# Kernel optimization log

Measured on AMD Instinct MI355X. Metric: run time of the kernel, lower is better.

## Reference

```python
import jax, jax.numpy as jnp
import numpy as np


def _gru_dirs(x, h, w_ih, w_hh, b_ih, b_hh):
    # One GRU step for both directions at once (seq_len==1 per original loop).
    # x: [N, in], h: [2, N, H]; w_ih: [2, 3H, in], w_hh: [2, 3H, H], biases [2, 3H]
    gi = jnp.einsum('ni,dgi->dng', x, w_ih) + b_ih[:, None, :]
    gh = jnp.einsum('dnh,dgh->dng', h, w_hh) + b_hh[:, None, :]
    H = h.shape[-1]
    ir, iz, inn = gi[..., :H], gi[..., H:2 * H], gi[..., 2 * H:]
    hr, hz, hn = gh[..., :H], gh[..., H:2 * H], gh[..., 2 * H:]
    r = jax.nn.sigmoid(ir + hr)
    z = jax.nn.sigmoid(iz + hz)
    n = jnp.tanh(inn + r * hn)
    return (1.0 - z) * n + z * h


def setup_inputs() -> dict:
    key = jax.random.key(0)
    ks = jax.random.split(key, 6)
    V, E, H, NL = 32000, 1024, 512, 2  # vocab, input_size, hidden_size, num_layers
    N, L = 32, 512
    s = 0.05
    x = jax.random.randint(ks[0], (N, L), 0, V)
    emb = jax.random.normal(ks[1], (V, E), dtype=jnp.float32) * s
    w_ih = jax.random.normal(ks[2], (NL, 2, 3 * H, E), dtype=jnp.float32) * s
    w_hh = jax.random.normal(ks[3], (NL, 2, 3 * H, H), dtype=jnp.float32) * s
    b_ih = jax.random.normal(ks[4], (NL, 2, 3 * H), dtype=jnp.float32) * s
    b_hh = jax.random.normal(ks[5], (NL, 2, 3 * H), dtype=jnp.float32) * s
    return {"x": x, "emb": emb, "w_ih": w_ih, "w_hh": w_hh, "b_ih": b_ih, "b_hh": b_hh}


def reference(x, emb, w_ih, w_hh, b_ih, b_hh):
    # Because the torch code calls the bidirectional GRU one timestep at a time
    # with a carried hidden, BOTH directions scan left-to-right over the sequence.
    N, L = x.shape
    num_layers = w_ih.shape[0]
    H = w_hh.shape[-1]
    h0 = jnp.zeros((num_layers, 2, N, H), dtype=emb.dtype)

    def step(h, xt):
        layer_in = emb[xt]  # [N, E] embedding lookup for this timestep
        new_h = []
        for l in range(num_layers):  # fixed small layer loop
            hl = _gru_dirs(layer_in, h[l], w_ih[l], w_hh[l], b_ih[l], b_hh[l])
            new_h.append(hl)
            layer_in = jnp.concatenate([hl[0], hl[1]], axis=-1)  # [N, 2H]
        hs = jnp.stack(new_h)  # [num_layers, 2, N, H]
        return hs, (layer_in, hs)

    _, (outs, hiddens) = jax.lax.scan(step, h0, x.T)  # scan over L timesteps
    outputs = jnp.transpose(outs, (1, 0, 2))  # [N, L, 2H]
    hiddens = hiddens.reshape(L, num_layers * 2, N, H)  # [L, 2*num_layers, N, H]
    return outputs, hiddens
```

## Files before the change

### kernel.cpp

```cpp
#include <hip/hip_runtime.h>
#include <hip/hip_bf16.h>

using u16 = unsigned short;
using u32 = unsigned int;
using bf16x8 = __attribute__((ext_vector_type(8))) __bf16;
using f32x4  = __attribute__((ext_vector_type(4))) float;

#define GLP(p) ((const __attribute__((address_space(1))) void*)(p))
#define LDSP(p) ((__attribute__((address_space(3))) void*)(p))

__device__ __forceinline__ float bf2f(u16 u) {
    union { float f; u32 i; } v; v.i = ((u32)u) << 16; return v.f;
}
__device__ __forceinline__ u16 f2bf(float f) {
    union { float f; u32 i; } v; v.f = f;
    u32 r = v.i + 0x7FFFu + ((v.i >> 16) & 1u);
    return (u16)(r >> 16);
}

__device__ __forceinline__ u32 ld_sc01_u32(const u32* p) {
    u32 v;
    asm volatile("global_load_dword %0, %1, off sc0 sc1\n\ts_waitcnt vmcnt(0)"
                 : "=v"(v) : "v"(p) : "memory");
    return v;
}
__device__ __forceinline__ void st_sc01_u32(u32* p, u32 v) {
    asm volatile("global_store_dword %0, %1, off sc0 sc1" :: "v"(p), "v"(v) : "memory");
}
__device__ __forceinline__ void st_sc01_u16(u16* p, u16 v) {
    asm volatile("global_store_short %0, %1, off sc0 sc1" :: "v"(p), "v"(v) : "memory");
}

__global__ void k_gather(const int* __restrict__ x, const float* __restrict__ emb,
                         u16* __restrict__ X0) {
    int gid = blockIdx.x * blockDim.x + threadIdx.x;
    if (gid >= 16384 * 256) return;
    int e4 = gid << 2;
    int m = e4 >> 10, k = e4 & 1023;
    int t = m >> 5, n = m & 31;
    int tok = x[n * 512 + t];
    float4 v = *reinterpret_cast<const float4*>(emb + ((size_t)tok << 10) + k);
    ushort4 o;
    o.x = f2bf(v.x); o.y = f2bf(v.y); o.z = f2bf(v.z); o.w = f2bf(v.w);
    *reinterpret_cast<ushort4*>(X0 + (size_t)e4) = o;
}

__global__ void k_f32bf16(const float* __restrict__ s, u16* __restrict__ d, int n4) {
    int gid = blockIdx.x * blockDim.x + threadIdx.x;
    if (gid >= n4) return;
    float4 v = reinterpret_cast<const float4*>(s)[gid];
    ushort4 o;
    o.x = f2bf(v.x); o.y = f2bf(v.y); o.z = f2bf(v.z); o.w = f2bf(v.w);
    reinterpret_cast<ushort4*>(d)[gid] = o;
}

__global__ __launch_bounds__(256) void k_gemm(const u16* __restrict__ A,
                                              const u16* __restrict__ B,
                                              const float* __restrict__ bias,
                                              u16* __restrict__ C,
                                              int M, int N, int K) {
    __shared__ __align__(16) u16 As[128 * 64];
    __shared__ __align__(16) u16 Bs[128 * 64];
    const int tid = threadIdx.x;
    const int lane = tid & 63, wid = tid >> 6;
    const int wm = wid >> 1, wn = wid & 1;
    const int m0 = blockIdx.y * 128, n0 = blockIdx.x * 128;
    const int lr = lane & 15, lk = lane >> 4;
    f32x4 zero = {0.f, 0.f, 0.f, 0.f};
    f32x4 acc[4][4];
    #pragma unroll
    for (int i = 0; i < 4; ++i)
        #pragma unroll
        for (int j = 0; j < 4; ++j) acc[i][j] = zero;

    for (int k0 = 0; k0 < K; k0 += 64) {
        #pragma unroll
        for (int r = 0; r < 4; ++r) {
            int c = wid * 4 + r;
            int o = c * 1024 + lane * 16;
            int row = o >> 7;
            int kb = o & 127;
            int kbs = kb ^ ((row & 7) << 4);
            const char* sa = (const char*)A + ((size_t)(m0 + row) * K + k0) * 2 + kbs;
            const char* sb = (const char*)B + ((size_t)(n0 + row) * K + k0) * 2 + kbs;
            __builtin_amdgcn_global_load_lds(GLP(sa), LDSP((char*)As + c * 1024), 16, 0, 0);
            __builtin_amdgcn_global_load_lds(GLP(sb), LDSP((char*)Bs + c * 1024), 16, 0, 0);
        }
        __syncthreads();
        #pragma unroll
        for (int kk = 0; kk < 2; ++kk) {
            bf16x8 af[4], bfr[4];
            #pragma unroll
            for (int i = 0; i < 4; ++i) {
                int rowA = wm * 64 + i * 16 + lr;
                int rowB = wn * 64 + i * 16 + lr;
                int kb = kk * 64 + lk * 16;
                af[i]  = *reinterpret_cast<const bf16x8*>((const char*)As + rowA * 128 + (kb ^ ((rowA & 7) << 4)));
                bfr[i] = *reinterpret_cast<const bf16x8*>((const char*)Bs + rowB * 128 + (kb ^ ((rowB & 7) << 4)));
            }
            #pragma unroll
            for (int i = 0; i < 4; ++i)
                #pragma unroll
                for (int j = 0; j < 4; ++j)
                    acc[i][j] = __builtin_amdgcn_mfma_f32_16x16x32_bf16(af[i], bfr[j], acc[i][j], 0, 0, 0);
        }
        __syncthreads();
    }
    #pragma unroll
    for (int j = 0; j < 4; ++j) {
        int col = n0 + wn * 64 + j * 16 + lr;
        float bv = bias[col];
        #pragma unroll
        for (int i = 0; i < 4; ++i) {
            int rowb = m0 + wm * 64 + i * 16 + lk * 4;
            #pragma unroll
            for (int q = 0; q < 4; ++q)
                C[(size_t)(rowb + q) * N + col] = f2bf(acc[i][j][q] + bv);
        }
    }
}

template<int LAYER>
__device__ __forceinline__ void gru_body(char* smem, int d, int wg,
    const u16* __restrict__ Gi, const u16* __restrict__ Whh_l,
    const float* __restrict__ bhh_l, u16* __restrict__ hbuf,
    u16* __restrict__ X1, float* __restrict__ hid, float* __restrict__ outp,
    u32* __restrict__ flags, u32* __restrict__ xflags, const u32* __restrict__ gdone)
{
    char* hS          = smem;
    float (*ghs)[196] = (float(*)[196])(smem + 32768);
    u16 (*gis)[208]   = (u16(*)[208])(smem + 57856);
    float* bhh_s      = (float*)(smem + 71168);
    const int tid = threadIdx.x;
    const int lane = tid & 63, w = tid >> 6;
    const int j0 = wg * 64;
    const int g = w >> 2, joff = (w & 3) * 16;
    const int lr = lane & 15, lk = lane >> 4;

    if (tid < 192) {
        int g2 = tid >> 6, jj = tid & 63;
        bhh_s[tid] = bhh_l[d * 1536 + g2 * 512 + j0 + jj];
    }
    bf16x8 wf[16];
    {
        const u16* wr = Whh_l + (size_t)(d * 1536 + g * 512 + j0 + joff + lr) * 512 + lk * 8;
        #pragma unroll
        for (int kt = 0; kt < 16; ++kt)
            wf[kt] = *reinterpret_cast<const bf16x8*>(wr + kt * 32);
    }
    if (LAYER == 1 && tid == 0) {
        long long T0 = __builtin_amdgcn_s_memrealtime();
        while (ld_sc01_u32(&gdone[0]) == 0) {
            __builtin_amdgcn_s_sleep(4);
            if (__builtin_amdgcn_s_memrealtime() - T0 > 2000000) break;
        }
    }
    __syncthreads();

    const int p_nb = tid / 24, p_gc = tid % 24;
    const int p_lg = p_gc * 8;
    const int p_col = d * 1536 + (p_lg >> 6) * 512 + j0 + (p_lg & 63);
    const u32* myflags = flags + d * 8 * 32;
    u32* myflag  = flags  + (d * 8 + wg) * 32;
    u32* myxflag = (LAYER == 0) ? xflags + (d * 8 + wg) * 32 : nullptr;

    float hp0 = 0.f, hp1 = 0.f, hp2 = 0.f;
    uint4 gv;
    if (LAYER == 0)
        gv = *reinterpret_cast<const uint4*>(Gi + (size_t)p_nb * 3072 + p_col);

    for (int t = 0; t < 512; ++t) {
        if (t > 0) {
            if (tid < 8) {
                const u32* fp = myflags + tid * 32;
                long long tt0 = __builtin_amdgcn_s_memrealtime();
                while (ld_sc01_u32(fp) < (u32)t) {
                    __builtin_amdgcn_s_sleep(1);
                    if (__builtin_amdgcn_s_memrealtime() - tt0 > 2000) {
                        __hip_atomic_store(myflag, (u32)t, __ATOMIC_RELEASE,
                                           __HIP_MEMORY_SCOPE_AGENT);
                        tt0 = __builtin_amdgcn_s_memrealtime();
                    }
                }
            } else if (LAYER == 1 && tid == 8) {
                long long tt0 = __builtin_amdgcn_s_memrealtime();
                while (ld_sc01_u32(&gdone[t >> 2]) == 0) {
                    __builtin_amdgcn_s_sleep(1);
                    if (__builtin_amdgcn_s_memrealtime() - tt0 > 2000000) break;
                }
            }
            __syncthreads();
        }

        const u16* hb = hbuf + ((size_t)d * 2 + ((t + 1) & 1)) * 16384;
        uint4 hv0, hv1, hv2;
        {
            int c0 = tid, c1 = tid + 768, c2 = tid + 1536;
            asm volatile("global_load_dwordx4 %0, %1, off sc0 sc1"
                         : "=v"(hv0) : "v"(hb + (size_t)(c0 >> 6) * 512 + (c0 & 63) * 8));
            asm volatile("global_load_dwordx4 %0, %1, off sc0 sc1"
                         : "=v"(hv1) : "v"(hb + (size_t)(c1 >> 6) * 512 + (c1 & 63) * 8));
            if (c2 < 2048)
                asm volatile("global_load_dwordx4 %0, %1, off sc0 sc1"
                             : "=v"(hv2) : "v"(hb + (size_t)(c2 >> 6) * 512 + (c2 & 63) * 8));
        }
        if (LAYER == 1) {
            const u16* gip = Gi + (size_t)(t * 32 + p_nb) * 3072 + p_col;
            asm volatile("global_load_dwordx4 %0, %1, off sc0 sc1" : "=v"(gv) : "v"(gip));
        }
        asm volatile("s_waitcnt vmcnt(0)" ::: "memory");
        {
            int c0 = tid, c1 = tid + 768, c2 = tid + 1536;
            int r0 = c0 >> 6, r1 = c1 >> 6, r2 = c2 >> 6;
            *reinterpret_cast<uint4*>(hS + r0 * 1024 + (((c0 & 63) * 16) ^ ((r0 & 15) << 4))) = hv0;
            *reinterpret_cast<uint4*>(hS + r1 * 1024 + (((c1 & 63) * 16) ^ ((r1 & 15) << 4))) = hv1;
            if (c2 < 2048)
                *reinterpret_cast<uint4*>(hS + r2 * 1024 + (((c2 & 63) * 16) ^ ((r2 & 15) << 4))) = hv2;
        }
        *reinterpret_cast<uint4*>(&gis[p_nb][p_lg]) = gv;
        __syncthreads();

        f32x4 acc0 = {0.f, 0.f, 0.f, 0.f}, acc1 = acc0;
        #pragma unroll
        for (int ktb = 0; ktb < 4; ++ktb) {
            bf16x8 a0[4], a1[4];
            #pragma unroll
            for (int r = 0; r < 4; ++r) {
                int kt = ktb * 4 + r;
                int boff = (lk * 16 + kt * 64) ^ (lr << 4);
                a0[r] = *reinterpret_cast<const bf16x8*>(hS + lr * 1024 + boff);
                a1[r] = *reinterpret_cast<const bf16x8*>(hS + (16 + lr) * 1024 + boff);
            }
            #pragma unroll
            for (int r = 0; r < 4; ++r) {
                acc0 = __builtin_amdgcn_mfma_f32_16x16x32_bf16(a0[r], wf[ktb * 4 + r], acc0, 0, 0, 0);
                acc1 = __builtin_amdgcn_mfma_f32_16x16x32_bf16(a1[r], wf[ktb * 4 + r], acc1, 0, 0, 0);
            }
        }
        int colg = w * 16 + lr;
        float bv = bhh_s[colg];
        #pragma unroll
        for (int q = 0; q < 4; ++q) {
            ghs[lk * 4 + q][colg]      = acc0[q] + bv;
            ghs[16 + lk * 4 + q][colg] = acc1[q] + bv;
        }
        if (LAYER == 0) {
            int tn = (t + 1 < 512) ? t + 1 : t;
            gv = *reinterpret_cast<const uint4*>(Gi + (size_t)(tn * 32 + p_nb) * 3072 + p_col);
        }
        __syncthreads();

        u16* hbw = hbuf + ((size_t)d * 2 + (t & 1)) * 16384;
        #pragma unroll
        for (int rep = 0; rep < 3; ++rep) {
            int e = tid + rep * 768;
            if (e < 2048) {
                int j = e & 63, nb = e >> 6;
                float gr = bf2f(gis[nb][j])       + ghs[nb][j];
                float gz = bf2f(gis[nb][64 + j])  + ghs[nb][64 + j];
                float r = 1.f / (1.f + __expf(-gr));
                float z = 1.f / (1.f + __expf(-gz));
                float ng = tanhf(bf2f(gis[nb][128 + j]) + r * ghs[nb][128 + j]);
                float hp = (rep == 0) ? hp0 : (rep == 1) ? hp1 : hp2;
                float hv = (1.f - z) * ng + z * hp;
                if (rep == 0) hp0 = hv; else if (rep == 1) hp1 = hv; else hp2 = hv;
                st_sc01_u16(hbw + (size_t)nb * 512 + j0 + j, f2bf(hv));
            }
        }
        asm volatile("s_waitcnt vmcnt(0)" ::: "memory");
        __syncthreads();
        if (tid == 0)
            st_sc01_u32(myflag, (u32)(t + 1));

        #pragma unroll
        for (int rep = 0; rep < 3; ++rep) {
            int e = tid + rep * 768;
            if (e < 2048) {
                int j = e & 63, nb = e >> 6;
                float hv = (rep == 0) ? hp0 : (rep == 1) ? hp1 : hp2;
                hid[((size_t)(t * 4 + LAYER * 2 + d) * 32 + nb) * 512 + j0 + j] = hv;
                if (LAYER == 0)
                    st_sc01_u16(X1 + ((size_t)(t * 32 + nb)) * 1024 + (size_t)d * 512 + j0 + j,
                                f2bf(hv));
                else
                    outp[((size_t)nb * 512 + t) * 1024 + (size_t)d * 512 + j0 + j] = hv;
            }
        }
        if (LAYER == 0) {
            asm volatile("s_waitcnt vmcnt(0)" ::: "memory");
            __syncthreads();
            if (tid == 0)
                st_sc01_u32(myxflag, (u32)(t + 1));
        }
    }
}

__device__ __forceinline__ void chaser_body(char* smem, int w,
    const u16* __restrict__ X1, const u16* __restrict__ Wih1,
    const float* __restrict__ bih1, u16* __restrict__ Gi,
    const u32* __restrict__ xflags, u32* __restrict__ cnt, u32* __restrict__ gdone)
{
    u16* As = (u16*)smem;
    u16* Bs = (u16*)(smem + 16384);
    const int tid = threadIdx.x;
    const int lane = tid & 63, wid = tid >> 6;
    const int wm = wid & 1, wn = wid >> 1;
    const int lr = lane & 15, lk = lane >> 4;
    const int x = w & 31, yg = w >> 5;

    for (int y = yg; y < 128; y += 3) {
        if (tid < 16) {
            const u32* fp = xflags + tid * 32;
            u32 target = 4u * (u32)y + 4u;
            long long T0 = __builtin_amdgcn_s_memrealtime();
            while (ld_sc01_u32(fp) < target) {
                __builtin_amdgcn_s_sleep(4);
                if (__builtin_amdgcn_s_memrealtime() - T0 > 2000000) break;
            }
        }
        __syncthreads();

        f32x4 zero = {0.f, 0.f, 0.f, 0.f};
        f32x4 acc[4][2];
        #pragma unroll
        for (int i = 0; i < 4; ++i) { acc[i][0] = zero; acc[i][1] = zero; }

        for (int k0 = 0; k0 < 1024; k0 += 64) {
            #pragma unroll
            for (int r = 0; r < 5; ++r) {
                int c = wid * 5 + r;
                if (c < 16) {
                    int o = c * 1024 + lane * 16;
                    int row = o >> 7, kb = o & 127;
                    int kbs = kb ^ ((row & 7) << 4);
                    const char* s = (const char*)X1 + ((size_t)(y * 128 + row) * 1024 + k0) * 2 + kbs;
                    __builtin_amdgcn_global_load_lds(GLP(s), LDSP((char*)As + c * 1024), 16, 0, 0);
                } else if (c < 28) {
                    int c2 = c - 16;
                    int o = c2 * 1024 + lane * 16;
                    int row = o >> 7, kb = o & 127;
                    int kbs = kb ^ ((row & 7) << 4);
                    const char* s = (const char*)Wih1 + ((size_t)(x * 96 + row) * 1024 + k0) * 2 + kbs;
                    __builtin_amdgcn_global_load_lds(GLP(s), LDSP((char*)Bs + c2 * 1024), 16, 0, 0);
                }
            }
            __syncthreads();
            if (wid < 6) {
                #pragma unroll
                for (int kk = 0; kk < 2; ++kk) {
                    bf16x8 af[4], bfr[2];
                    int kb = kk * 64 + lk * 16;
                    #pragma unroll
                    for (int i = 0; i < 4; ++i) {
                        int rowA = wm * 64 + i * 16 + lr;
                        af[i] = *reinterpret_cast<const bf16x8*>((const char*)As + rowA * 128 + (kb ^ ((rowA & 7) << 4)));
                    }
                    #pragma unroll
                    for (int j = 0; j < 2; ++j) {
                        int rowB = wn * 32 + j * 16 + lr;
                        bfr[j] = *reinterpret_cast<const bf16x8*>((const char*)Bs + rowB * 128 + (kb ^ ((rowB & 7) << 4)));
                    }
                    #pragma unroll
                    for (int i = 0; i < 4; ++i)
                        #pragma unroll
                        for (int j = 0; j < 2; ++j)
                            acc[i][j] = __builtin_amdgcn_mfma_f32_16x16x32_bf16(af[i], bfr[j], acc[i][j], 0, 0, 0);
                }
            }
            __syncthreads();
        }
        if (wid < 6) {
            #pragma unroll
            for (int j = 0; j < 2; ++j) {
                int col = x * 96 + wn * 32 + j * 16 + lr;
                float bv = bih1[col];
                #pragma unroll
                for (int i = 0; i < 4; ++i) {
                    int rowb = y * 128 + wm * 64 + i * 16 + lk * 4;
                    #pragma unroll
                    for (int q = 0; q < 4; ++q)
                        st_sc01_u16(Gi + (size_t)(rowb + q) * 3072 + col, f2bf(acc[i][j][q] + bv));
                }
            }
        }
        asm volatile("s_waitcnt vmcnt(0)" ::: "memory");
        __syncthreads();
        if (tid == 0) {
            u32 old = __hip_atomic_fetch_add(&cnt[y], 1u, __ATOMIC_RELAXED,
                                             __HIP_MEMORY_SCOPE_AGENT);
            if (old == 31u)
                st_sc01_u32(&gdone[y], 1u);
        }
    }
}

__global__ __launch_bounds__(768, 3) void k_fused(
    const u16* __restrict__ Gi_r, u16* __restrict__ Gi_w,
    const u16* __restrict__ Whh, const float* __restrict__ bhh,
    u16* __restrict__ hbuf0, u16* __restrict__ hbuf1,
    u16* __restrict__ X1, const u16* __restrict__ Wih1, const float* __restrict__ bih1,
    float* __restrict__ hid, float* __restrict__ outp,
    u32* __restrict__ flags0, u32* __restrict__ flags1,
    u32* __restrict__ xflags, u32* __restrict__ cnt, u32* __restrict__ gdone)
{
    __shared__ __align__(16) char smem[71936];
    int bid = blockIdx.x;
    if (bid < 16) {
        gru_body<0>(smem, bid >> 3, bid & 7, Gi_r, Whh, bhh, hbuf0,
                    X1, hid, outp, flags0, xflags, nullptr);
    } else if (bid < 112) {
        chaser_body(smem, bid - 16, X1, Wih1, bih1, Gi_w, xflags, cnt, gdone);
    } else {
        int b = bid - 112;
        gru_body<1>(smem, b >> 3, b & 7, Gi_r, Whh + (size_t)3072 * 512, bhh + 3072,
                    hbuf1, nullptr, hid, outp, flags1, nullptr, gdone);
    }
}

extern "C" void kernel_launch(void* const* d_in, const int* in_sizes, int n_in,
                              void* d_out, int out_size, void* d_ws, size_t ws_size,
                              hipStream_t stream) {
    const int*   x    = (const int*)d_in[0];
    const float* emb  = (const float*)d_in[1];
    const float* w_ih = (const float*)d_in[2];
    const float* w_hh = (const float*)d_in[3];
    const float* b_ih = (const float*)d_in[4];
    const float* b_hh = (const float*)d_in[5];
    float* outp = (float*)d_out;
    float* hid  = outp + (size_t)32 * 512 * 1024;

    char* ws = (char*)d_ws;
    u16* X0     = (u16*)(ws);
    u16* X1     = (u16*)(ws + 33554432);
    u16* Wih    = (u16*)(ws + 67108864);
    u16* Whh    = (u16*)(ws + 79691776);
    u16* Gi     = (u16*)(ws + 85983232);
    u16* hbuf0  = (u16*)(ws + 186646528);
    u16* hbuf1  = (u16*)(ws + 186777600);
    u32* flags0 = (u32*)(ws + 186908672);
    u32* flags1 = (u32*)(ws + 186910720);
    u32* xflags = (u32*)(ws + 186912768);
    u32* cnt    = (u32*)(ws + 186914816);
    u32* gdone  = (u32*)(ws + 186915328);

    k_gather<<<16384, 256, 0, stream>>>(x, emb, X0);
    k_f32bf16<<<(1572864 + 255) / 256, 256, 0, stream>>>(w_ih, Wih, 1572864);
    k_f32bf16<<<( 786432 + 255) / 256, 256, 0, stream>>>(w_hh, Whh, 786432);

    hipMemsetAsync(hbuf0, 0, 269312, stream);

    k_gemm<<<dim3(24, 128), 256, 0, stream>>>(X0, Wih, b_ih, Gi, 16384, 3072, 1024);

    k_fused<<<128, 768, 0, stream>>>(Gi, Gi, Whh, b_hh, hbuf0, hbuf1,
                                     X1, Wih + (size_t)3072 * 1024, b_ih + 3072,
                                     hid, outp, flags0, flags1, xflags, cnt, gdone);
}
```

Before: 2.396 ms.

## Split hidden-state load to overlap MFMA with loads and vectorize output stores

```diff
diff --git a/kernel.cpp b/kernel.cpp
--- a/kernel.cpp
+++ b/kernel.cpp
@@ -5,6 +5,7 @@
 using u32 = unsigned int;
 using bf16x8 = __attribute__((ext_vector_type(8))) __bf16;
 using f32x4  = __attribute__((ext_vector_type(4))) float;
+using u32x4  = __attribute__((ext_vector_type(4))) u32;
 
 #define GLP(p) ((const __attribute__((address_space(1))) void*)(p))
 #define LDSP(p) ((__attribute__((address_space(3))) void*)(p))
@@ -29,6 +30,9 @@
 }
 __device__ __forceinline__ void st_sc01_u16(u16* p, u16 v) {
     asm volatile("global_store_short %0, %1, off sc0 sc1" :: "v"(p), "v"(v) : "memory");
+}
+__device__ __forceinline__ void st_sc01_u32x4(u16* p, u32x4 v) {
+    asm volatile("global_store_dwordx4 %0, %1, off sc0 sc1" :: "v"(p), "v"(v) : "memory");
 }
 
 __global__ void k_gather(const int* __restrict__ x, const float* __restrict__ emb,
@@ -131,6 +135,7 @@
     float (*ghs)[196] = (float(*)[196])(smem + 32768);
     u16 (*gis)[208]   = (u16(*)[208])(smem + 57856);
     float* bhh_s      = (float*)(smem + 71168);
+    u16* hvS          = (u16*)(smem + 71936);
     const int tid = threadIdx.x;
     const int lane = tid & 63, w = tid >> 6;
     const int j0 = wg * 64;
@@ -163,6 +168,10 @@
     const u32* myflags = flags + d * 8 * 32;
     u32* myflag  = flags  + (d * 8 + wg) * 32;
     u32* myxflag = (LAYER == 0) ? xflags + (d * 8 + wg) * 32 : nullptr;
+
+    const int srow = tid >> 6;
+    const int scol = (tid & 63) * 8;
+    const int scb  = (tid & 63) * 16;
 
     float hp0 = 0.f, hp1 = 0.f, hp2 = 0.f;
     uint4 gv;
@@ -193,49 +202,58 @@
         }
 
         const u16* hb = hbuf + ((size_t)d * 2 + ((t + 1) & 1)) * 16384;
-        uint4 hv0, hv1, hv2;
-        {
-            int c0 = tid, c1 = tid + 768, c2 = tid + 1536;
+        u32x4 va0, va1, vb0, vb1, gvv;
+        if (tid < 512) {
             asm volatile("global_load_dwordx4 %0, %1, off sc0 sc1"
-                         : "=v"(hv0) : "v"(hb + (size_t)(c0 >> 6) * 512 + (c0 & 63) * 8));
+                         : "=v"(va0) : "v"(hb + (size_t)srow * 512 + scol));
             asm volatile("global_load_dwordx4 %0, %1, off sc0 sc1"
-                         : "=v"(hv1) : "v"(hb + (size_t)(c1 >> 6) * 512 + (c1 & 63) * 8));
-            if (c2 < 2048)
-                asm volatile("global_load_dwordx4 %0, %1, off sc0 sc1"
-                             : "=v"(hv2) : "v"(hb + (size_t)(c2 >> 6) * 512 + (c2 & 63) * 8));
+                         : "=v"(va1) : "v"(hb + (size_t)(srow + 8) * 512 + scol));
+            asm volatile("global_load_dwordx4 %0, %1, off sc0 sc1"
+                         : "=v"(vb0) : "v"(hb + (size_t)(srow + 16) * 512 + scol));
+            asm volatile("global_load_dwordx4 %0, %1, off sc0 sc1"
+                         : "=v"(vb1) : "v"(hb + (size_t)(srow + 24) * 512 + scol));
         }
         if (LAYER == 1) {
             const u16* gip = Gi + (size_t)(t * 32 + p_nb) * 3072 + p_col;
-            asm volatile("global_load_dwordx4 %0, %1, off sc0 sc1" : "=v"(gv) : "v"(gip));
-        }
-        asm volatile("s_waitcnt vmcnt(0)" ::: "memory");
-        {
-            int c0 = tid, c1 = tid + 768, c2 = tid + 1536;
-            int r0 = c0 >> 6, r1 = c1 >> 6, r2 = c2 >> 6;
-            *reinterpret_cast<uint4*>(hS + r0 * 1024 + (((c0 & 63) * 16) ^ ((r0 & 15) << 4))) = hv0;
-            *reinterpret_cast<uint4*>(hS + r1 * 1024 + (((c1 & 63) * 16) ^ ((r1 & 15) << 4))) = hv1;
-            if (c2 < 2048)
-                *reinterpret_cast<uint4*>(hS + r2 * 1024 + (((c2 & 63) * 16) ^ ((r2 & 15) << 4))) = hv2;
-        }
-        *reinterpret_cast<uint4*>(&gis[p_nb][p_lg]) = gv;
-        __syncthreads();
-
-        f32x4 acc0 = {0.f, 0.f, 0.f, 0.f}, acc1 = acc0;
-        #pragma unroll
-        for (int ktb = 0; ktb < 4; ++ktb) {
-            bf16x8 a0[4], a1[4];
-            #pragma unroll
-            for (int r = 0; r < 4; ++r) {
-                int kt = ktb * 4 + r;
-                int boff = (lk * 16 + kt * 64) ^ (lr << 4);
-                a0[r] = *reinterpret_cast<const bf16x8*>(hS + lr * 1024 + boff);
-                a1[r] = *reinterpret_cast<const bf16x8*>(hS + (16 + lr) * 1024 + boff);
-            }
-            #pragma unroll
-            for (int r = 0; r < 4; ++r) {
-                acc0 = __builtin_amdgcn_mfma_f32_16x16x32_bf16(a0[r], wf[ktb * 4 + r], acc0, 0, 0, 0);
-                acc1 = __builtin_amdgcn_mfma_f32_16x16x32_bf16(a1[r], wf[ktb * 4 + r], acc1, 0, 0, 0);
-            }
+            asm volatile("global_load_dwordx4 %0, %1, off sc0 sc1" : "=v"(gvv) : "v"(gip));
+        }
+        if (tid < 512) {
+            if (LAYER == 0) asm volatile("s_waitcnt vmcnt(2)" ::: "memory");
+            else            asm volatile("s_waitcnt vmcnt(3)" ::: "memory");
+            int r0 = srow, r1 = srow + 8;
+            *reinterpret_cast<u32x4*>(hS + r0 * 1024 + (scb ^ ((r0 & 15) << 4))) = va0;
+            *reinterpret_cast<u32x4*>(hS + r1 * 1024 + (scb ^ ((r1 & 15) << 4))) = va1;
+        }
+        __syncthreads();
+
+        f32x4 acc0 = {0.f, 0.f, 0.f, 0.f};
+        #pragma unroll
+        for (int kt = 0; kt < 16; ++kt) {
+            int boff = (lk * 16 + kt * 64) ^ (lr << 4);
+            bf16x8 a = *reinterpret_cast<const bf16x8*>(hS + lr * 1024 + boff);
+            acc0 = __builtin_amdgcn_mfma_f32_16x16x32_bf16(a, wf[kt], acc0, 0, 0, 0);
+        }
+        if (tid < 512) {
+            asm volatile("s_waitcnt vmcnt(0)" ::: "memory");
+            int r2 = srow + 16, r3 = srow + 24;
+            *reinterpret_cast<u32x4*>(hS + r2 * 1024 + (scb ^ ((r2 & 15) << 4))) = vb0;
+            *reinterpret_cast<u32x4*>(hS + r3 * 1024 + (scb ^ ((r3 & 15) << 4))) = vb1;
+        } else if (LAYER == 1) {
+            asm volatile("s_waitcnt vmcnt(0)" ::: "memory");
+        }
+        if (LAYER == 0) {
+            *reinterpret_cast<uint4*>(&gis[p_nb][p_lg]) = gv;
+        } else {
+            *reinterpret_cast<u32x4*>(&gis[p_nb][p_lg]) = gvv;
+        }
+        __syncthreads();
+
+        f32x4 acc1 = {0.f, 0.f, 0.f, 0.f};
+        #pragma unroll
+        for (int kt = 0; kt < 16; ++kt) {
+            int boff = (lk * 16 + kt * 64) ^ (lr << 4);
+            bf16x8 a = *reinterpret_cast<const bf16x8*>(hS + (16 + lr) * 1024 + boff);
+            acc1 = __builtin_amdgcn_mfma_f32_16x16x32_bf16(a, wf[kt], acc1, 0, 0, 0);
         }
         int colg = w * 16 + lr;
         float bv = bhh_s[colg];
@@ -264,32 +282,38 @@
                 float hp = (rep == 0) ? hp0 : (rep == 1) ? hp1 : hp2;
                 float hv = (1.f - z) * ng + z * hp;
                 if (rep == 0) hp0 = hv; else if (rep == 1) hp1 = hv; else hp2 = hv;
-                st_sc01_u16(hbw + (size_t)nb * 512 + j0 + j, f2bf(hv));
+                u16 hb16 = f2bf(hv);
+                st_sc01_u16(hbw + (size_t)nb * 512 + j0 + j, hb16);
+                hvS[nb * 64 + j] = hb16;
             }
         }
         asm volatile("s_waitcnt vmcnt(0)" ::: "memory");
         __syncthreads();
-        if (tid == 0)
+        if (tid == 16)
             st_sc01_u32(myflag, (u32)(t + 1));
 
-        #pragma unroll
-        for (int rep = 0; rep < 3; ++rep) {
-            int e = tid + rep * 768;
-            if (e < 2048) {
-                int j = e & 63, nb = e >> 6;
-                float hv = (rep == 0) ? hp0 : (rep == 1) ? hp1 : hp2;
-                hid[((size_t)(t * 4 + LAYER * 2 + d) * 32 + nb) * 512 + j0 + j] = hv;
-                if (LAYER == 0)
-                    st_sc01_u16(X1 + ((size_t)(t * 32 + nb)) * 1024 + (size_t)d * 512 + j0 + j,
-                                f2bf(hv));
-                else
-                    outp[((size_t)nb * 512 + t) * 1024 + (size_t)d * 512 + j0 + j] = hv;
-            }
-        }
-        if (LAYER == 0) {
+        if (tid >= 512) {
+            int q = tid - 512, nb = q >> 3, j8 = (q & 7) * 8;
+            union { u32x4 v; u16 s[8]; } h8;
+            h8.v = *reinterpret_cast<const u32x4*>(hvS + nb * 64 + j8);
+            float f0 = bf2f(h8.s[0]), f1 = bf2f(h8.s[1]), f2 = bf2f(h8.s[2]), f3 = bf2f(h8.s[3]);
+            float f4 = bf2f(h8.s[4]), f5 = bf2f(h8.s[5]), f6 = bf2f(h8.s[6]), f7 = bf2f(h8.s[7]);
+            float* hp = hid + ((size_t)(t * 4 + LAYER * 2 + d) * 32 + nb) * 512 + j0 + j8;
+            *reinterpret_cast<float4*>(hp)     = make_float4(f0, f1, f2, f3);
+            *reinterpret_cast<float4*>(hp + 4) = make_float4(f4, f5, f6, f7);
+            if (LAYER == 0) {
+                u16* xp = X1 + (size_t)(t * 32 + nb) * 1024 + (size_t)d * 512 + j0 + j8;
+                st_sc01_u32x4(xp, h8.v);
+            } else {
+                float* op = outp + ((size_t)nb * 512 + t) * 1024 + (size_t)d * 512 + j0 + j8;
+                *reinterpret_cast<float4*>(op)     = make_float4(f0, f1, f2, f3);
+                *reinterpret_cast<float4*>(op + 4) = make_float4(f4, f5, f6, f7);
+            }
+        }
+        if (LAYER == 0 && (t & 3) == 3) {
             asm volatile("s_waitcnt vmcnt(0)" ::: "memory");
             __syncthreads();
-            if (tid == 0)
+            if (tid == 17)
                 st_sc01_u32(myxflag, (u32)(t + 1));
         }
     }
@@ -403,7 +427,7 @@
     u32* __restrict__ flags0, u32* __restrict__ flags1,
     u32* __restrict__ xflags, u32* __restrict__ cnt, u32* __restrict__ gdone)
 {
-    __shared__ __align__(16) char smem[71936];
+    __shared__ __align__(16) char smem[76032];
     int bid = blockIdx.x;
     if (bid < 16) {
         gru_body<0>(smem, bid >> 3, bid & 7, Gi_r, Whh, bhh, hbuf0,
@@ -447,7 +471,7 @@
     k_f32bf16<<<(1572864 + 255) / 256, 256, 0, stream>>>(w_ih, Wih, 1572864);
     k_f32bf16<<<( 786432 + 255) / 256, 256, 0, stream>>>(w_hh, Whh, 786432);
 
-    hipMemsetAsync(hbuf0, 0, 269312, stream);
+    (void)hipMemsetAsync(hbuf0, 0, 269312, stream);
 
     k_gemm<<<dim3(24, 128), 256, 0, stream>>>(X0, Wih, b_ih, Gi, 16384, 3072, 1024);
 
```

New measurement: 2.271 ms. -5.2%, faster.
